# Kernel optimization log

Measured on AMD Instinct MI355X. Metric: run time of the kernel, lower is better.

## Reference

```python
import jax, jax.numpy as jnp
import numpy as np

H = 1024        # hidden_size
E = 16          # n_routed_experts
K = 4           # num_experts_per_tok (top_k)
I = 512         # moe_intermediate_size
NS = 2          # n_shared_experts
IS = I * NS     # shared-expert intermediate size
N = 2048        # num_tokens
ROUTED_SCALE = 2.5  # routed_scaling_factor


def setup_inputs() -> dict:
    key = jax.random.key(0)
    ks = jax.random.split(key, 6)
    s = 0.02
    return {
        "hidden_states": jax.random.normal(ks[0], (N, H), jnp.float32),
        "gate_w": jax.random.normal(ks[1], (H, E), jnp.float32) * s,
        "w_gate_up": jax.random.normal(ks[2], (E, H, 2 * I), jnp.float32) * s,
        "w_down": jax.random.normal(ks[3], (E, I, H), jnp.float32) * s,
        "shared_gate_up": jax.random.normal(ks[4], (H, 2 * IS), jnp.float32) * s,
        "shared_down": jax.random.normal(ks[5], (IS, H), jnp.float32) * s,
    }


def _moe_forward(x, gate_w, w_gate_up, w_down, shared_gate_up, shared_down):
    n = x.shape[0]
    # --- router: sigmoid scoring + top-k (num_expert_group=topk_group=1) ---
    router_logits = x @ gate_w                      # [N, E]
    scores = jax.nn.sigmoid(router_logits)
    top_vals, top_idx = jax.lax.top_k(scores, K)    # [N, K]
    # renormalize (norm_topk_prob=True)
    top_w = top_vals / jnp.sum(top_vals, axis=-1, keepdims=True)
    # dense combine weights [N, E], zero outside top-k
    w_dense = jnp.zeros((n, E), x.dtype).at[jnp.arange(n)[:, None], top_idx].add(top_w)

    # --- routed experts: SwiGLU per expert, weighted combine ---
    gu = jnp.einsum("nh,ehf->nef", x, w_gate_up)    # [N, E, 2I]
    act = jax.nn.silu(gu[..., :I]) * gu[..., I:]    # SiluAndMul -> [N, E, I]
    routed = jnp.einsum("nei,eih,ne->nh", act, w_down, w_dense)  # [N, H]

    # --- shared experts MLP (WBLMLP) ---
    gus = x @ shared_gate_up                        # [N, 2*IS]
    shared = (jax.nn.silu(gus[:, :IS]) * gus[:, IS:]) @ shared_down  # [N, H]

    return routed * ROUTED_SCALE + shared


def reference(hidden_states, gate_w, w_gate_up, w_down, shared_gate_up, shared_down):
    return _moe_forward(hidden_states, gate_w, w_gate_up, w_down,
                        shared_gate_up, shared_down)
```

## Files before the change

### kernel.cpp

```cpp
#include <hip/hip_runtime.h>
#include <hip/hip_bf16.h>
#include <stdint.h>

#define NTOK 2048
#define HDIM 1024
#define NEXP 16
#define TOPK 4
#define IR   512
#define ISH  1024
#define RSCALE 2.5f

typedef short bf16x4 __attribute__((ext_vector_type(4)));
typedef short bf16x8 __attribute__((ext_vector_type(8)));
typedef float f32x4  __attribute__((ext_vector_type(4)));

static __device__ __forceinline__ unsigned short f2bf(float f){
  union { float fv; uint32_t u; } v; v.fv = f;
  uint32_t r = v.u + 0x7fffu + ((v.u >> 16) & 1u);
  return (unsigned short)(r >> 16);
}
static __device__ __forceinline__ float bf2f(unsigned short s){
  union { uint32_t u; float f; } v; v.u = ((uint32_t)s) << 16;
  return v.f;
}
static __device__ __forceinline__ unsigned int pkbf2(float lo, float hi){
  union { __hip_bfloat162 b; unsigned int u; } cv;
  cv.b = __float22bfloat162_rn(make_float2(lo, hi));
  return cv.u;
}

static __device__ __forceinline__ void gl_lds16(const void* gp, void* lp){
  __builtin_amdgcn_global_load_lds(
      (const __attribute__((address_space(1))) unsigned int*)gp,
      (__attribute__((address_space(3))) unsigned int*)lp, 16, 0, 0);
}


static __device__ __forceinline__ void conv_tile(
    const float* __restrict__ s, unsigned short* __restrict__ d,
    int R, int C, int rt, int ct, int tid, float* tile)
{
  const int r0 = rt * 64, c0 = ct * 64;
  #pragma unroll
  for (int i = 0; i < 4; i++){
    int r = i * 16 + (tid >> 4);
    int c = (tid & 15) * 4;
    float4 v = *(const float4*)(s + (size_t)(r0 + r) * C + c0 + c);
    *(float4*)(tile + r * 69 + c) = v;
  }
  __syncthreads();
  unsigned short* dt = d + ((size_t)ct * (R >> 6) + rt) * 4096;
  #pragma unroll
  for (int it = 0; it < 2; it++){
    int q = tid + it * 256;
    int c = q >> 3, rg = (q & 7) * 8;
    union { bf16x8 v; unsigned int u[4]; } pk;
    #pragma unroll
    for (int k = 0; k < 4; k++)
      pk.u[k] = pkbf2(tile[(rg + 2 * k) * 69 + c], tile[(rg + 2 * k + 1) * 69 + c]);
    *(bf16x8*)(dt + c * 64 + rg) = pk.v;
  }
}

__global__ __launch_bounds__(256) void prep_kernel(
    const float* __restrict__ x, const float* __restrict__ gw,
    float* __restrict__ topkw, int* __restrict__ choice,
    unsigned short* __restrict__ xbf,
    const float* __restrict__ wgu, unsigned short* __restrict__ wgu_t,
    const float* __restrict__ sgu, unsigned short* __restrict__ sgu_t)
{
  __shared__ __align__(16) float tile[64 * 69];
  const int tid = threadIdx.x;
  const int bid = blockIdx.x;

  if (bid < 512){
    const int lane = tid & 63;
    const int t = bid * 4 + (tid >> 6);
    float s[NEXP];
    #pragma unroll
    for (int e = 0; e < NEXP; e++) s[e] = 0.f;
    #pragma unroll
    for (int j = 0; j < 8; j++){
      const int off = 128 * j + lane * 2;
      float2 xv = *(const float2*)(x + (size_t)t * HDIM + off);
      ushort2 xs = { f2bf(xv.x), f2bf(xv.y) };
      *(ushort2*)(xbf + (size_t)t * HDIM + off) = xs;
      const float4* g0 = (const float4*)(gw + (size_t)off * NEXP);
      const float4* g1 = (const float4*)(gw + (size_t)(off + 1) * NEXP);
      #pragma unroll
      for (int q = 0; q < 4; q++){
        float4 a = g0[q], b = g1[q];
        s[q * 4 + 0] += xv.x * a.x + xv.y * b.x;
        s[q * 4 + 1] += xv.x * a.y + xv.y * b.y;
        s[q * 4 + 2] += xv.x * a.z + xv.y * b.z;
        s[q * 4 + 3] += xv.x * a.w + xv.y * b.w;
      }
    }
    #pragma unroll
    for (int e = 0; e < NEXP; e++){
      #pragma unroll
      for (int off = 32; off; off >>= 1)
        s[e] += __shfl_xor(s[e], off);
    }
    float sc[NEXP];
    #pragma unroll
    for (int e = 0; e < NEXP; e++) sc[e] = 1.f / (1.f + __expf(-s[e]));
    unsigned mask = 0; float w[TOPK]; int id[TOPK];
    #pragma unroll
    for (int k = 0; k < TOPK; k++){
      float best = -1e30f; int bi = 0;
      #pragma unroll
      for (int e = 0; e < NEXP; e++){
        if (!((mask >> e) & 1u) && sc[e] > best){ best = sc[e]; bi = e; }
      }
      mask |= 1u << bi; id[k] = bi; w[k] = best;
    }
    float inv = 1.f / (w[0] + w[1] + w[2] + w[3]);
    if (lane == 0){
      #pragma unroll
      for (int k = 0; k < TOPK; k++){
        topkw[t * TOPK + k] = w[k] * inv;
        choice[t * TOPK + k] = id[k];
      }
    }
    return;
  }

  int id = bid - 512;
  if (id < 4096){
    int e = id >> 8, r = id & 255;
    conv_tile(wgu + (size_t)e * 1048576, wgu_t + (size_t)e * 1048576,
              1024, 1024, r >> 4, r & 15, tid, tile);
  } else {
    id -= 4096;
    conv_tile(sgu, sgu_t, 1024, 2048, id >> 5, id & 31, tid, tile);
  }
}

__global__ __launch_bounds__(256) void build_lists(
    const int* __restrict__ choice, int* __restrict__ counts, int* __restrict__ lists)
{
  const int e = blockIdx.x;
  const int tid = threadIdx.x;
  __shared__ int scnt[256];
  const int base = tid * 32;
  unsigned m = 0; int local = 0;
  #pragma unroll
  for (int i = 0; i < 32; i++){
    bool hit = (choice[base + i] == e);
    m |= (unsigned)hit << i;
    local += hit;
  }
  scnt[tid] = local;
  __syncthreads();
  int v = local;
  for (int off = 1; off < 256; off <<= 1){
    int add = (tid >= off) ? scnt[tid - off] : 0;
    __syncthreads();
    v += add; scnt[tid] = v;
    __syncthreads();
  }
  int pos = v - local;
  #pragma unroll
  for (int i = 0; i < 32; i++){
    if ((m >> i) & 1u) lists[e * NTOK + pos++] = base + i;
  }
  if (tid == 255) counts[e] = v;
}

__global__ __launch_bounds__(256) void gu_plus(
    const unsigned short* __restrict__ xbf, const unsigned short* __restrict__ wgu_t,
    const unsigned short* __restrict__ sgu_t,
    unsigned short* __restrict__ act_r, unsigned short* __restrict__ act_s,
    const int* __restrict__ lists, const int* __restrict__ counts,
    const float* __restrict__ wdn, unsigned short* __restrict__ wdn_t,
    const float* __restrict__ sdn, unsigned short* __restrict__ sdn_t)
{
  __shared__ __align__(16) char smem[33280];
  const int tid = threadIdx.x;
  const int L = blockIdx.x;

  if (L >= 768){
    float* tile = (float*)smem;
    int id = L - 768;
    if (id < 2048){
      int e = id >> 7, r = id & 127;
      conv_tile(wdn + (size_t)e * 524288, wdn_t + (size_t)e * 524288,
                512, 1024, r >> 4, r & 15, tid, tile);
    } else {
      id -= 2048;
      conv_tile(sdn, sdn_t, 1024, 1024, id >> 4, id & 15, tid, tile);
    }
    return;
  }

  unsigned short* sA0 = (unsigned short*)smem;
  unsigned short* sA1 = sA0 + 4096;
  unsigned short* sB0 = sA1 + 4096;
  unsigned short* sB1 = sB0 + 4096;
  int* sAid = (int*)(smem + 32768);

  const bool routed = (L < 512);
  int e, mIdx, n0, count, NPAIR, NCH;
  const unsigned short* Bt;
  unsigned short* act;
  if (routed){
    int p = L & 7, t = L >> 3;
    mIdx = t & 3; e = t >> 2; n0 = p * 64;
    count = counts[e]; NPAIR = IR; NCH = 4;
    Bt = wgu_t + (size_t)e * (2 * IR) * HDIM;
    act = act_r;
  } else {
    int v = L - 512;
    e = 0; n0 = (v & 15) * 64; mIdx = v >> 4;
    count = NTOK; NPAIR = ISH; NCH = 16;
    Bt = sgu_t; act = act_s;
  }

  const int wv = tid >> 6, lane = tid & 63, lr = lane & 15, g = lane >> 4;
  const int wm = wv >> 1, wn = wv & 1;

  const unsigned short* bsrc[2];
  #pragma unroll
  for (int it = 0; it < 2; it++){
    int q = tid + it * 256;
    int c = q >> 2, ko = (q & 3) * 8;
    int grp = c >> 5, within = c & 31;
    int grow = n0 + (grp >> 1) * 32 + within + ((grp & 1) ? NPAIR : 0);
    bsrc[it] = Bt + ((size_t)(grow >> 6) * (HDIM >> 6)) * 4096 + ((grow & 63) << 6) + ko;
  }

  for (int mt = mIdx; mt * 128 < count; mt += NCH){
    const int m0 = mt * 128;
    __syncthreads();
    if (tid < 128){
      int idx = m0 + tid;
      int aid;
      if (routed) aid = (idx < count) ? lists[e * NTOK + idx] : lists[e * NTOK];
      else        aid = idx;
      sAid[tid] = aid;
    }
    __syncthreads();
    const unsigned short* asrc[2];
    #pragma unroll
    for (int it = 0; it < 2; it++){
      int q = tid + it * 256;
      int r = q >> 2, ko = (q & 3) * 8;
      int aid = sAid[r];
      int tok = routed ? (aid >> 2) : aid;
      asrc[it] = xbf + (size_t)tok * HDIM + ko;
    }

    const f32x4 z4 = {0.f, 0.f, 0.f, 0.f};
    f32x4 acc[4][4];
    #pragma unroll
    for (int i = 0; i < 4; i++)
      #pragma unroll
      for (int j = 0; j < 4; j++) acc[i][j] = z4;

    for (int k0 = 0; k0 < HDIM; k0 += 64){
      const size_t bk = (size_t)k0 * 64;
      #pragma unroll
      for (int it = 0; it < 2; it++){
        gl_lds16(asrc[it] + k0,       sA0 + (tid + it * 256) * 8);
        gl_lds16(asrc[it] + k0 + 32,  sA1 + (tid + it * 256) * 8);
        gl_lds16(bsrc[it] + bk,       sB0 + (tid + it * 256) * 8);
        gl_lds16(bsrc[it] + bk + 32,  sB1 + (tid + it * 256) * 8);
      }
      __syncthreads();
      #pragma unroll
      for (int h = 0; h < 2; h++){
        const unsigned short* sAh = h ? sA1 : sA0;
        const unsigned short* sBh = h ? sB1 : sB0;
        bf16x8 af[4], bfr[4];
        #pragma unroll
        for (int i = 0; i < 4; i++){
          af[i]  = *(const bf16x8*)(sAh + (wm * 64 + i * 16 + lr) * 32 + g * 8);
          bfr[i] = *(const bf16x8*)(sBh + (wn * 64 + i * 16 + lr) * 32 + g * 8);
        }
        #pragma unroll
        for (int mi = 0; mi < 4; mi++)
          #pragma unroll
          for (int ni = 0; ni < 4; ni++)
            acc[mi][ni] = __builtin_amdgcn_mfma_f32_16x16x32_bf16(af[mi], bfr[ni], acc[mi][ni], 0, 0, 0);
      }
      __syncthreads();
    }

    #pragma unroll
    for (int mi = 0; mi < 4; mi++){
      #pragma unroll
      for (int r = 0; r < 4; r++){
        int row = wm * 64 + mi * 16 + g * 4 + r;
        if (routed && m0 + row >= count) continue;
        int aid = sAid[row];
        size_t arow = (size_t)aid * NPAIR;
        #pragma unroll
        for (int ni = 0; ni < 2; ni++){
          float gv = acc[mi][ni][r];
          float uv = acc[mi][ni + 2][r];
          float a = gv / (1.f + __expf(-gv)) * uv;
          act[arow + n0 + wn * 32 + ni * 16 + lr] = f2bf(a);
        }
      }
    }
  }
}

__global__ __launch_bounds__(256) void down_gemm(
    const unsigned short* __restrict__ act_r, const unsigned short* __restrict__ act_s,
    const unsigned short* __restrict__ wdn_t, const unsigned short* __restrict__ sdn_t,
    float* __restrict__ out, unsigned short* __restrict__ downout,
    const int* __restrict__ lists, const int* __restrict__ counts)
{
  __shared__ unsigned short sA[2][128 * 32];
  __shared__ unsigned short sB[2][128 * 32];
  __shared__ int sAid[128];

  const int tid = threadIdx.x;
  const int L = blockIdx.x;
  const bool routed = (L < 512);
  int e, mIdx, n0, count, K, NCH;
  const unsigned short* Bt;
  const unsigned short* Ab;
  if (routed){
    int p = L & 7, t = L >> 3;
    mIdx = t & 3; e = t >> 2; n0 = p * 128;
    count = counts[e]; K = IR; NCH = 4;
    Bt = wdn_t + (size_t)e * HDIM * IR;
    Ab = act_r;
  } else {
    int v = L - 512;
    e = 0; n0 = (v & 7) * 128; mIdx = v >> 3;
    count = NTOK; K = ISH; NCH = 16;
    Bt = sdn_t; Ab = act_s;
  }

  const int wv = tid >> 6, lane = tid & 63, lr = lane & 15, g = lane >> 4;
  const int wm = wv >> 1, wn = wv & 1;

  const unsigned short* bsrc[2];
  #pragma unroll
  for (int it = 0; it < 2; it++){
    int q = tid + it * 256;
    int c = q >> 2, ko = (q & 3) * 8;
    int grow = n0 + c;
    bsrc[it] = Bt + ((size_t)(grow >> 6) * (K >> 6)) * 4096 + ((grow & 63) << 6) + ko;
  }

  for (int mt = mIdx; mt * 128 < count; mt += NCH){
    const int m0 = mt * 128;
    __syncthreads();
    if (tid < 128){
      int idx = m0 + tid;
      int aid;
      if (routed) aid = (idx < count) ? lists[e * NTOK + idx] : lists[e * NTOK];
      else        aid = idx;
      sAid[tid] = aid;
    }
    __syncthreads();
    const unsigned short* asrc[2];
    #pragma unroll
    for (int it = 0; it < 2; it++){
      int q = tid + it * 256;
      int r = q >> 2, ko = (q & 3) * 8;
      asrc[it] = Ab + (size_t)sAid[r] * K + ko;
    }

    const f32x4 z4 = {0.f, 0.f, 0.f, 0.f};
    f32x4 acc[4][4];
    #pragma unroll
    for (int i = 0; i < 4; i++)
      #pragma unroll
      for (int j = 0; j < 4; j++) acc[i][j] = z4;

    for (int k0 = 0; k0 < K; k0 += 64){
      const size_t bk = (size_t)k0 * 64;
      #pragma unroll
      for (int it = 0; it < 2; it++){
        gl_lds16(asrc[it] + k0,       sA[0] + (tid + it * 256) * 8);
        gl_lds16(asrc[it] + k0 + 32,  sA[1] + (tid + it * 256) * 8);
        gl_lds16(bsrc[it] + bk,       sB[0] + (tid + it * 256) * 8);
        gl_lds16(bsrc[it] + bk + 32,  sB[1] + (tid + it * 256) * 8);
      }
      __syncthreads();
      #pragma unroll
      for (int h = 0; h < 2; h++){
        bf16x8 af[4], bfr[4];
        #pragma unroll
        for (int i = 0; i < 4; i++){
          af[i]  = *(const bf16x8*)(sA[h] + (wm * 64 + i * 16 + lr) * 32 + g * 8);
          bfr[i] = *(const bf16x8*)(sB[h] + (wn * 64 + i * 16 + lr) * 32 + g * 8);
        }
        #pragma unroll
        for (int mi = 0; mi < 4; mi++)
          #pragma unroll
          for (int ni = 0; ni < 4; ni++)
            acc[mi][ni] = __builtin_amdgcn_mfma_f32_16x16x32_bf16(af[mi], bfr[ni], acc[mi][ni], 0, 0, 0);
      }
      __syncthreads();
    }

    #pragma unroll
    for (int mi = 0; mi < 4; mi++){
      #pragma unroll
      for (int r = 0; r < 4; r++){
        int row = wm * 64 + mi * 16 + g * 4 + r;
        if (m0 + row >= count) continue;
        int aid = sAid[row];
        size_t orow = (size_t)aid * HDIM;
        if (routed){
          #pragma unroll
          for (int ni = 0; ni < 4; ni++)
            downout[orow + n0 + wn * 64 + ni * 16 + lr] = f2bf(acc[mi][ni][r]);
        } else {
          #pragma unroll
          for (int ni = 0; ni < 4; ni++)
            out[orow + n0 + wn * 64 + ni * 16 + lr] = acc[mi][ni][r];
        }
      }
    }
  }
}

__global__ __launch_bounds__(256) void combine_kernel(
    float* __restrict__ out, const unsigned short* __restrict__ downout,
    const float* __restrict__ topkw)
{
  const int idx = blockIdx.x * 256 + threadIdx.x;
  const int t = idx >> 8;
  const int c4 = (idx & 255) * 4;
  float4 o = *(float4*)(out + (size_t)t * HDIM + c4);
  float r0 = 0.f, r1 = 0.f, r2 = 0.f, r3 = 0.f;
  #pragma unroll
  for (int k = 0; k < TOPK; k++){
    float w = topkw[t * TOPK + k];
    const ushort4 dv = *(const ushort4*)(downout + (size_t)(t * TOPK + k) * HDIM + c4);
    r0 += w * bf2f(dv.x); r1 += w * bf2f(dv.y);
    r2 += w * bf2f(dv.z); r3 += w * bf2f(dv.w);
  }
  o.x += RSCALE * r0; o.y += RSCALE * r1; o.z += RSCALE * r2; o.w += RSCALE * r3;
  *(float4*)(out + (size_t)t * HDIM + c4) = o;
}

extern "C" void kernel_launch(void* const* d_in, const int* in_sizes, int n_in,
                              void* d_out, int out_size, void* d_ws, size_t ws_size,
                              hipStream_t stream) {
  const float* x   = (const float*)d_in[0];
  const float* gw  = (const float*)d_in[1];
  const float* wgu = (const float*)d_in[2];
  const float* wdn = (const float*)d_in[3];
  const float* sgu = (const float*)d_in[4];
  const float* sdn = (const float*)d_in[5];
  float* out = (float*)d_out;

  char* ws = (char*)d_ws;
  float* topkw = (float*)(ws + 0);
  int* choice  = (int*)(ws + 32768);
  int* counts  = (int*)(ws + 65536);
  int* lists   = (int*)(ws + 65792);
  unsigned short* xbf   = (unsigned short*)(ws + 197120);
  unsigned short* wgu_t = (unsigned short*)(ws + 197120 + 4194304ull);
  unsigned short* wdn_t = (unsigned short*)(ws + 197120 + 37748736ull);
  unsigned short* sgu_t = (unsigned short*)(ws + 197120 + 54525952ull);
  unsigned short* sdn_t = (unsigned short*)(ws + 197120 + 58720256ull);
  unsigned short* act_r = (unsigned short*)(ws + 197120 + 60817408ull);
  unsigned short* act_s = (unsigned short*)(ws + 197120 + 69206016ull);
  unsigned short* downout = wgu_t;

  prep_kernel<<<512 + 4608, 256, 0, stream>>>(x, gw, topkw, choice, xbf,
                                              wgu, wgu_t, sgu, sgu_t);
  build_lists<<<NEXP, 256, 0, stream>>>(choice, counts, lists);
  gu_plus<<<768 + 2304, 256, 0, stream>>>(xbf, wgu_t, sgu_t, act_r, act_s,
                                          lists, counts, wdn, wdn_t, sdn, sdn_t);
  down_gemm<<<640, 256, 0, stream>>>(act_r, act_s, wdn_t, sdn_t, out, downout, lists, counts);
  combine_kernel<<<(NTOK * HDIM / 4) / 256, 256, 0, stream>>>(out, downout, topkw);
}
```

Baseline: 129.6 us.

## Convert two weight tiles per block and split shared down-GEMM K across blocks

```diff
diff --git a/kernel.cpp b/kernel.cpp
--- a/kernel.cpp
+++ b/kernel.cpp
@@ -36,29 +36,40 @@
 }
 
 
-static __device__ __forceinline__ void conv_tile(
+static __device__ __forceinline__ void conv_tile2(
     const float* __restrict__ s, unsigned short* __restrict__ d,
-    int R, int C, int rt, int ct, int tid, float* tile)
-{
-  const int r0 = rt * 64, c0 = ct * 64;
+    int R, int C, int rt0, int ct, int tid, float* t0, float* t1)
+{
+  const int c0 = ct * 64;
+  const int rr = tid >> 4, cc = (tid & 15) * 4;
+  float4 v0[4], v1[4];
   #pragma unroll
   for (int i = 0; i < 4; i++){
-    int r = i * 16 + (tid >> 4);
-    int c = (tid & 15) * 4;
-    float4 v = *(const float4*)(s + (size_t)(r0 + r) * C + c0 + c);
-    *(float4*)(tile + r * 69 + c) = v;
+    int r = i * 16 + rr;
+    v0[i] = *(const float4*)(s + (size_t)(rt0 * 64 + r) * C + c0 + cc);
+    v1[i] = *(const float4*)(s + (size_t)(rt0 * 64 + 64 + r) * C + c0 + cc);
+  }
+  #pragma unroll
+  for (int i = 0; i < 4; i++){
+    int r = i * 16 + rr;
+    *(float4*)(t0 + r * 69 + cc) = v0[i];
+    *(float4*)(t1 + r * 69 + cc) = v1[i];
   }
   __syncthreads();
-  unsigned short* dt = d + ((size_t)ct * (R >> 6) + rt) * 4096;
-  #pragma unroll
-  for (int it = 0; it < 2; it++){
-    int q = tid + it * 256;
-    int c = q >> 3, rg = (q & 7) * 8;
-    union { bf16x8 v; unsigned int u[4]; } pk;
-    #pragma unroll
-    for (int k = 0; k < 4; k++)
-      pk.u[k] = pkbf2(tile[(rg + 2 * k) * 69 + c], tile[(rg + 2 * k + 1) * 69 + c]);
-    *(bf16x8*)(dt + c * 64 + rg) = pk.v;
+  #pragma unroll
+  for (int h = 0; h < 2; h++){
+    const float* tile = h ? t1 : t0;
+    unsigned short* dt = d + ((size_t)ct * (R >> 6) + rt0 + h) * 4096;
+    #pragma unroll
+    for (int it = 0; it < 2; it++){
+      int q = tid + it * 256;
+      int c = q >> 3, rg = (q & 7) * 8;
+      union { bf16x8 v; unsigned int u[4]; } pk;
+      #pragma unroll
+      for (int k = 0; k < 4; k++)
+        pk.u[k] = pkbf2(tile[(rg + 2 * k) * 69 + c], tile[(rg + 2 * k + 1) * 69 + c]);
+      *(bf16x8*)(dt + c * 64 + rg) = pk.v;
+    }
   }
 }
 
@@ -69,7 +80,7 @@
     const float* __restrict__ wgu, unsigned short* __restrict__ wgu_t,
     const float* __restrict__ sgu, unsigned short* __restrict__ sgu_t)
 {
-  __shared__ __align__(16) float tile[64 * 69];
+  __shared__ __align__(16) float tiles[2][64 * 69];
   const int tid = threadIdx.x;
   const int bid = blockIdx.x;
 
@@ -127,13 +138,13 @@
   }
 
   int id = bid - 512;
-  if (id < 4096){
-    int e = id >> 8, r = id & 255;
-    conv_tile(wgu + (size_t)e * 1048576, wgu_t + (size_t)e * 1048576,
-              1024, 1024, r >> 4, r & 15, tid, tile);
+  if (id < 2048){
+    int e = id >> 7, j = id & 127;
+    conv_tile2(wgu + (size_t)e * 1048576, wgu_t + (size_t)e * 1048576,
+               1024, 1024, (j >> 4) * 2, j & 15, tid, tiles[0], tiles[1]);
   } else {
-    id -= 4096;
-    conv_tile(sgu, sgu_t, 1024, 2048, id >> 5, id & 31, tid, tile);
+    id -= 2048;
+    conv_tile2(sgu, sgu_t, 1024, 2048, (id >> 5) * 2, id & 31, tid, tiles[0], tiles[1]);
   }
 }
 
@@ -176,20 +187,21 @@
     const float* __restrict__ wdn, unsigned short* __restrict__ wdn_t,
     const float* __restrict__ sdn, unsigned short* __restrict__ sdn_t)
 {
-  __shared__ __align__(16) char smem[33280];
+  __shared__ __align__(16) char smem[35328];
   const int tid = threadIdx.x;
   const int L = blockIdx.x;
 
   if (L >= 768){
-    float* tile = (float*)smem;
+    float* t0 = (float*)smem;
+    float* t1 = t0 + 64 * 69;
     int id = L - 768;
-    if (id < 2048){
-      int e = id >> 7, r = id & 127;
-      conv_tile(wdn + (size_t)e * 524288, wdn_t + (size_t)e * 524288,
-                512, 1024, r >> 4, r & 15, tid, tile);
+    if (id < 1024){
+      int e = id >> 6, j = id & 63;
+      conv_tile2(wdn + (size_t)e * 524288, wdn_t + (size_t)e * 524288,
+                 512, 1024, (j >> 4) * 2, j & 15, tid, t0, t1);
     } else {
-      id -= 2048;
-      conv_tile(sdn, sdn_t, 1024, 1024, id >> 4, id & 15, tid, tile);
+      id -= 1024;
+      conv_tile2(sdn, sdn_t, 1024, 1024, (id >> 4) * 2, id & 15, tid, t0, t1);
     }
     return;
   }
@@ -310,7 +322,7 @@
 __global__ __launch_bounds__(256) void down_gemm(
     const unsigned short* __restrict__ act_r, const unsigned short* __restrict__ act_s,
     const unsigned short* __restrict__ wdn_t, const unsigned short* __restrict__ sdn_t,
-    float* __restrict__ out, unsigned short* __restrict__ downout,
+    float* __restrict__ shout, unsigned short* __restrict__ downout,
     const int* __restrict__ lists, const int* __restrict__ counts)
 {
   __shared__ unsigned short sA[2][128 * 32];
@@ -320,20 +332,23 @@
   const int tid = threadIdx.x;
   const int L = blockIdx.x;
   const bool routed = (L < 512);
-  int e, mIdx, n0, count, K, NCH;
+  int e, mIdx, n0, count, kBeg, kEnd, NCH, KT;
   const unsigned short* Bt;
   const unsigned short* Ab;
+  float* outp = nullptr;
   if (routed){
     int p = L & 7, t = L >> 3;
     mIdx = t & 3; e = t >> 2; n0 = p * 128;
-    count = counts[e]; K = IR; NCH = 4;
+    count = counts[e]; kBeg = 0; kEnd = IR; KT = IR; NCH = 4;
     Bt = wdn_t + (size_t)e * HDIM * IR;
     Ab = act_r;
   } else {
     int v = L - 512;
-    e = 0; n0 = (v & 7) * 128; mIdx = v >> 3;
-    count = NTOK; K = ISH; NCH = 16;
+    int half = v >> 7, w = v & 127;
+    e = 0; n0 = (w & 7) * 128; mIdx = w >> 3;
+    count = NTOK; kBeg = half * 512; kEnd = kBeg + 512; KT = ISH; NCH = 16;
     Bt = sdn_t; Ab = act_s;
+    outp = shout + (size_t)half * 2097152;
   }
 
   const int wv = tid >> 6, lane = tid & 63, lr = lane & 15, g = lane >> 4;
@@ -345,7 +360,7 @@
     int q = tid + it * 256;
     int c = q >> 2, ko = (q & 3) * 8;
     int grow = n0 + c;
-    bsrc[it] = Bt + ((size_t)(grow >> 6) * (K >> 6)) * 4096 + ((grow & 63) << 6) + ko;
+    bsrc[it] = Bt + ((size_t)(grow >> 6) * (KT >> 6)) * 4096 + ((grow & 63) << 6) + ko;
   }
 
   for (int mt = mIdx; mt * 128 < count; mt += NCH){
@@ -364,7 +379,7 @@
     for (int it = 0; it < 2; it++){
       int q = tid + it * 256;
       int r = q >> 2, ko = (q & 3) * 8;
-      asrc[it] = Ab + (size_t)sAid[r] * K + ko;
+      asrc[it] = Ab + (size_t)sAid[r] * KT + ko;
     }
 
     const f32x4 z4 = {0.f, 0.f, 0.f, 0.f};
@@ -374,7 +389,7 @@
       #pragma unroll
       for (int j = 0; j < 4; j++) acc[i][j] = z4;
 
-    for (int k0 = 0; k0 < K; k0 += 64){
+    for (int k0 = kBeg; k0 < kEnd; k0 += 64){
       const size_t bk = (size_t)k0 * 64;
       #pragma unroll
       for (int it = 0; it < 2; it++){
@@ -416,7 +431,7 @@
         } else {
           #pragma unroll
           for (int ni = 0; ni < 4; ni++)
-            out[orow + n0 + wn * 64 + ni * 16 + lr] = acc[mi][ni][r];
+            outp[orow + n0 + wn * 64 + ni * 16 + lr] = acc[mi][ni][r];
         }
       }
     }
@@ -424,13 +439,14 @@
 }
 
 __global__ __launch_bounds__(256) void combine_kernel(
-    float* __restrict__ out, const unsigned short* __restrict__ downout,
-    const float* __restrict__ topkw)
+    float* __restrict__ out, const float* __restrict__ shout,
+    const unsigned short* __restrict__ downout, const float* __restrict__ topkw)
 {
   const int idx = blockIdx.x * 256 + threadIdx.x;
   const int t = idx >> 8;
   const int c4 = (idx & 255) * 4;
-  float4 o = *(float4*)(out + (size_t)t * HDIM + c4);
+  float4 o0 = *(const float4*)(shout + (size_t)t * HDIM + c4);
+  float4 o1 = *(const float4*)(shout + 2097152 + (size_t)t * HDIM + c4);
   float r0 = 0.f, r1 = 0.f, r2 = 0.f, r3 = 0.f;
   #pragma unroll
   for (int k = 0; k < TOPK; k++){
@@ -439,7 +455,11 @@
     r0 += w * bf2f(dv.x); r1 += w * bf2f(dv.y);
     r2 += w * bf2f(dv.z); r3 += w * bf2f(dv.w);
   }
-  o.x += RSCALE * r0; o.y += RSCALE * r1; o.z += RSCALE * r2; o.w += RSCALE * r3;
+  float4 o;
+  o.x = o0.x + o1.x + RSCALE * r0;
+  o.y = o0.y + o1.y + RSCALE * r1;
+  o.z = o0.z + o1.z + RSCALE * r2;
+  o.w = o0.w + o1.w + RSCALE * r3;
   *(float4*)(out + (size_t)t * HDIM + c4) = o;
 }
 
@@ -467,12 +487,13 @@
   unsigned short* act_r = (unsigned short*)(ws + 197120 + 60817408ull);
   unsigned short* act_s = (unsigned short*)(ws + 197120 + 69206016ull);
   unsigned short* downout = wgu_t;
-
-  prep_kernel<<<512 + 4608, 256, 0, stream>>>(x, gw, topkw, choice, xbf,
+  float*          shout   = (float*)((char*)wgu_t + 16777216ull);
+
+  prep_kernel<<<512 + 2304, 256, 0, stream>>>(x, gw, topkw, choice, xbf,
                                               wgu, wgu_t, sgu, sgu_t);
   build_lists<<<NEXP, 256, 0, stream>>>(choice, counts, lists);
-  gu_plus<<<768 + 2304, 256, 0, stream>>>(xbf, wgu_t, sgu_t, act_r, act_s,
+  gu_plus<<<768 + 1152, 256, 0, stream>>>(xbf, wgu_t, sgu_t, act_r, act_s,
                                           lists, counts, wdn, wdn_t, sdn, sdn_t);
-  down_gemm<<<640, 256, 0, stream>>>(act_r, act_s, wdn_t, sdn_t, out, downout, lists, counts);
-  combine_kernel<<<(NTOK * HDIM / 4) / 256, 256, 0, stream>>>(out, downout, topkw);
-}
+  down_gemm<<<768, 256, 0, stream>>>(act_r, act_s, wdn_t, sdn_t, shout, downout, lists, counts);
+  combine_kernel<<<(NTOK * HDIM / 4) / 256, 256, 0, stream>>>(out, shout, downout, topkw);
+}
```

After: 125.1 us, median of 3. -3.4%, faster.
